# Performance work log

Hardware: AMD Instinct MI355X
Metric: run time of the kernel (lower is better)

The kernel has to match this reference:

```python
import jax, jax.numpy as jnp
import numpy as np

BT, NQ, NC, C, H, HID = 192, 64, 1024, 384, 8, 1536
DH = C // H                       # 48
SCALE = DH ** -0.5
MAX_NEG = -float(np.finfo(np.float32).max)


def _ln(x, eps, g=None, b=None):
    m = x.mean(-1, keepdims=True)
    v = ((x - m) ** 2).mean(-1, keepdims=True)
    y = (x - m) / jnp.sqrt(v + eps)
    if g is not None:
        y = y * g + b
    return y


def _gelu_tanh(x):
    # GELU(approximate='tanh')
    return 0.5 * x * (1.0 + jnp.tanh(jnp.sqrt(2.0 / jnp.pi) * (x + 0.044715 * x ** 3)))


def setup_inputs() -> dict:
    key = jax.random.key(0)
    ks = jax.random.split(key, 10)
    s = lambda fan: 1.0 / np.sqrt(fan)
    return {
        "x": jax.random.normal(ks[0], (BT, NQ, C), jnp.float32),
        "context": jax.random.normal(ks[1], (BT, NC, C), jnp.float32),
        "mask": jax.random.randint(ks[2], (BT, NQ), 0, 2) > 0,
        "Wq": jax.random.normal(ks[3], (C, C), jnp.float32) * s(C),
        "bq": jnp.zeros((C,), jnp.float32),
        "Wkv": jax.random.normal(ks[4], (C, 2 * C), jnp.float32) * s(C),
        "bkv": jnp.zeros((2 * C,), jnp.float32),
        "Wo": jax.random.normal(ks[5], (C, C), jnp.float32) * s(C),
        "bo": jnp.zeros((C,), jnp.float32),
        "g_ctx": jnp.ones((C,), jnp.float32),
        "b_ctx": jnp.zeros((C,), jnp.float32),
        "W1": jax.random.normal(ks[6], (C, HID), jnp.float32) * s(C),
        "b1": jnp.zeros((HID,), jnp.float32),
        "W2": jax.random.normal(ks[7], (HID, C), jnp.float32) * s(HID),
        "b2": jnp.zeros((C,), jnp.float32),
    }


def reference(x, context, mask, Wq, bq, Wkv, bkv, Wo, bo, g_ctx, b_ctx, W1, b1, W2, b2):
    # --- cross-attention branch ---
    xn = _ln(x, 1e-6)                       # norm1 (no affine)
    cn = _ln(context, 1e-5, g_ctx, b_ctx)   # norm_context (affine, default eps)
    q = (xn @ Wq + bq).reshape(BT, NQ, H, DH).transpose(0, 2, 1, 3)    # (B,H,NQ,DH)
    kv = cn @ Wkv + bkv
    k, v = jnp.split(kv, 2, axis=-1)
    k = k.reshape(BT, NC, H, DH).transpose(0, 2, 1, 3)                 # (B,H,NC,DH)
    v = v.reshape(BT, NC, H, DH).transpose(0, 2, 1, 3)
    sim = jnp.einsum('bhqd,bhkd->bhqk', q, k) * SCALE                  # (B,H,NQ,NC)
    # mask shape (BT, NQ): True = keep query row; ~mask * (-max) bias
    bias = jnp.where(mask[:, None, :, None], 0.0, MAX_NEG)
    attn = jax.nn.softmax(sim + bias, axis=-1)
    o = jnp.einsum('bhqk,bhkd->bhqd', attn, v).transpose(0, 2, 1, 3).reshape(BT, NQ, C)
    x = x + o @ Wo + bo
    # --- MLP branch ---
    xn2 = _ln(x, 1e-6)                      # norm2 (no affine)
    x = x + _gelu_tanh(xn2 @ W1 + b1) @ W2 + b2
    return x
```

## Files before the change

kernel.cpp:

```cpp
#include <hip/hip_runtime.h>
#include <hip/hip_bf16.h>
#include <math.h>

typedef unsigned int  u32;
typedef unsigned short u16;
typedef unsigned char u8;

#define BTn   192
#define NQn   64
#define NCn   1024
#define Cd    384
#define Hn    8
#define DHn   48
#define HIDn  1536
#define ROWSX (BTn*NQn)
#define ROWSC (BTn*NCn)
#define ATT_SCALE 0.14433756729740643f
#define CBc   64

typedef __bf16 bf16x8 __attribute__((ext_vector_type(8)));
typedef float  f32x4  __attribute__((ext_vector_type(4)));

#define GLL16(gp, lp) __builtin_amdgcn_global_load_lds( \
    (const __attribute__((address_space(1))) void*)(gp), \
    (__attribute__((address_space(3))) void*)(lp), 16, 0, 0)

__device__ __forceinline__ float bf2f(u32 u) {
  union { u32 i; float f; } v; v.i = u << 16; return v.f;
}
__device__ __forceinline__ u16 f2bf(float f) {
  union { float f; u32 i; } v; v.f = f;
  u32 x = v.i;
  x += 0x7fffu + ((x >> 16) & 1u);
  return (u16)(x >> 16);
}
__device__ __forceinline__ void decode8(uint4 r, float* v) {
  v[0]=bf2f(r.x & 0xffffu); v[1]=bf2f(r.x >> 16);
  v[2]=bf2f(r.y & 0xffffu); v[3]=bf2f(r.y >> 16);
  v[4]=bf2f(r.z & 0xffffu); v[5]=bf2f(r.z >> 16);
  v[6]=bf2f(r.w & 0xffffu); v[7]=bf2f(r.w >> 16);
}
__device__ __forceinline__ float gelu_f(float x) {
  float x3 = x*x*x;
  float z = 0.7978845608028654f*x + 0.035677408136300125f*x3;
  float e = __expf(2.f*z);
  float th = 1.f - 2.f/(e+1.f);
  return 0.5f*x*(1.f+th);
}

__global__ void decode_mask_kernel(const u8* __restrict__ m, u8* __restrict__ keep) {
  __shared__ int flags[3];
  int t = threadIdx.x;
  if (t < 3) flags[t] = 0;
  __syncthreads();
  int nonbin = 0, oddset = 0, low01 = 0;
  for (int i = t; i < ROWSX; i += 256) {
    u32 b = m[i];
    if (b > 1u) nonbin = 1;
    if ((i & 3) && b) oddset = 1;
    if (((i & 3) < 2) && b) low01 = 1;
  }
  if (nonbin) flags[0] = 1;
  if (oddset) flags[1] = 1;
  if (low01)  flags[2] = 1;
  __syncthreads();
  int mode = flags[0] ? (flags[2] ? 2 : 3) : (flags[1] ? 1 : 0);
  for (int i = t; i < ROWSX; i += 256) {
    u8 k;
    if (mode == 2)      k = (m[2*i] | m[2*i+1]) ? 1 : 0;
    else if (mode == 3) k = (((const float*)m)[i] != 0.f) ? 1 : 0;
    else if (mode == 1) k = m[i] ? 1 : 0;
    else                k = (((const int*)m)[i] != 0) ? 1 : 0;
    keep[i] = k;
  }
}

template<int AFF, int SRCF32>
__global__ __launch_bounds__(256) void lnorm_kernel(
    const void* __restrict__ srcv, const float* __restrict__ gw,
    const float* __restrict__ bw, u16* __restrict__ dst, float eps)
{
  const int row  = blockIdx.x * 4 + (threadIdx.x >> 6);
  const int lane = threadIdx.x & 63;
  float v[6];
  if (SRCF32) {
    const float2* p = (const float2*)((const float*)srcv + (size_t)row*Cd);
    #pragma unroll
    for (int i = 0; i < 3; i++) { float2 u = p[lane + 64*i]; v[2*i]=u.x; v[2*i+1]=u.y; }
  } else {
    const u32* p = (const u32*)((const u16*)srcv + (size_t)row*Cd);
    #pragma unroll
    for (int i = 0; i < 3; i++) { u32 u = p[lane + 64*i]; v[2*i]=bf2f(u&0xffffu); v[2*i+1]=bf2f(u>>16); }
  }
  float s  = v[0]+v[1]+v[2]+v[3]+v[4]+v[5];
  float s2 = v[0]*v[0]+v[1]*v[1]+v[2]*v[2]+v[3]*v[3]+v[4]*v[4]+v[5]*v[5];
  #pragma unroll
  for (int o = 32; o >= 1; o >>= 1) { s += __shfl_xor(s, o); s2 += __shfl_xor(s2, o); }
  float mean = s * (1.0f/Cd);
  float var  = s2 * (1.0f/Cd) - mean*mean;
  var = var > 0.f ? var : 0.f;
  float rstd = rsqrtf(var + eps);
  u32* d32 = (u32*)(dst + (size_t)row*Cd);
  #pragma unroll
  for (int i = 0; i < 3; i++) {
    float y0 = (v[2*i]   - mean) * rstd;
    float y1 = (v[2*i+1] - mean) * rstd;
    if (AFF) {
      float2 gg = *(const float2*)(gw + 2*(lane + 64*i));
      float2 bb = *(const float2*)(bw + 2*(lane + 64*i));
      y0 = y0*gg.x + bb.x;
      y1 = y1*gg.y + bb.y;
    }
    d32[lane + 64*i] = (u32)f2bf(y0) | ((u32)f2bf(y1) << 16);
  }
}

__global__ __launch_bounds__(256) void wconvt_kernel(
    const float* __restrict__ W, u16* __restrict__ WT, int K, int N)
{
  __shared__ u16 tile[64][66];
  const int t  = threadIdx.x;
  const int nt = N >> 6;
  const int bk = blockIdx.x / nt, bn = blockIdx.x % nt;
  const int q  = t >> 6;
  const int nl = t & 63;
  #pragma unroll
  for (int r = 0; r < 16; r++) {
    int k = q*16 + r;
    tile[nl][k] = f2bf(W[(size_t)(bk*64 + k)*N + bn*64 + nl]);
  }
  __syncthreads();
  #pragma unroll
  for (int r = 0; r < 16; r++) {
    int n = q*16 + r;
    WT[(size_t)(bn*64 + n)*K + bk*64 + nl] = tile[n][nl];
  }
}

template<int GEL, int RES, int RF32, int OF32>
__global__ __launch_bounds__(256) void mgemm_kernel(
    const u16* __restrict__ A, const u16* __restrict__ WT,
    const float* __restrict__ bias, const void* __restrict__ resv,
    void* __restrict__ Coutv, int M, int N, int K, int nx)
{
  __shared__ u16 As[3][4096];
  __shared__ u16 Bs[3][4096];
  const int t = threadIdx.x;
  const int w = t >> 6, l = t & 63, l15 = l & 15, g = l >> 4;

  const int nwg = gridDim.x;
  const int bid = blockIdx.x;
  const int wg  = (bid & 7) * (nwg >> 3) + (bid >> 3);
  const int n0 = (wg % nx) * 128, m0 = (wg / nx) * 128;
  const int wm = (w & 1) * 64, wn = (w >> 1) * 64;

  const int arow = t >> 2;
  const int swk  = (t >> 3) & 3;
  const int acol = ((t & 3) ^ swk) * 8;
  const u16* Ag = A  + (size_t)(m0 + arow) * K + acol;
  const u16* Wg = WT + (size_t)(n0 + arow) * K + acol;
  const size_t rowskip = (size_t)64 * K;

  const int xk   = (l15 >> 1) & 3;
  const int goff = ((g ^ xk) << 3);

  f32x4 acc[4][4];
  #pragma unroll
  for (int i = 0; i < 4; i++)
    #pragma unroll
    for (int j = 0; j < 4; j++) acc[i][j] = (f32x4){0.f, 0.f, 0.f, 0.f};

  const int nIter = K >> 5;

#define STAGE(nb, kk) do { \
    GLL16(Ag + (kk),           &As[nb][t*8]); \
    GLL16(Ag + (kk) + rowskip, &As[nb][2048 + t*8]); \
    GLL16(Wg + (kk),           &Bs[nb][t*8]); \
    GLL16(Wg + (kk) + rowskip, &Bs[nb][2048 + t*8]); \
  } while (0)

#define BODY(BUF, IT) do { \
    const int it_ = (IT); \
    if (it_ + 2 < nIter) { \
      STAGE((BUF + 2) % 3, (it_ + 2) << 5); \
      asm volatile("s_waitcnt vmcnt(8)" ::: "memory"); \
    } else if (it_ + 1 < nIter) { \
      asm volatile("s_waitcnt vmcnt(4)" ::: "memory"); \
    } else { \
      asm volatile("s_waitcnt vmcnt(0)" ::: "memory"); \
    } \
    __builtin_amdgcn_s_barrier(); \
    __builtin_amdgcn_sched_barrier(0); \
    { \
      bf16x8 af[4], bfv[4]; \
      _Pragma("unroll") \
      for (int i = 0; i < 4; i++) \
        af[i] = *(const bf16x8*)&As[BUF][(wm + i*16 + l15)*32 + goff]; \
      _Pragma("unroll") \
      for (int j = 0; j < 4; j++) \
        bfv[j] = *(const bf16x8*)&Bs[BUF][(wn + j*16 + l15)*32 + goff]; \
      _Pragma("unroll") \
      for (int i = 0; i < 4; i++) \
        _Pragma("unroll") \
        for (int j = 0; j < 4; j++) \
          acc[i][j] = __builtin_amdgcn_mfma_f32_16x16x32_bf16(bfv[j], af[i], acc[i][j], 0, 0, 0); \
    } \
    __builtin_amdgcn_sched_barrier(0); \
    __builtin_amdgcn_s_barrier(); \
  } while (0)

  STAGE(0, 0);
  STAGE(1, 32);
  for (int it0 = 0; it0 < nIter; it0 += 3) {
    BODY(0, it0);
    BODY(1, it0 + 1);
    BODY(2, it0 + 2);
  }
#undef BODY
#undef STAGE

  const float* resf = (const float*)resv;
  const u16*   resb = (const u16*)resv;
  float* Cf = (float*)Coutv;
  u16*   Cb = (u16*)Coutv;
  #pragma unroll
  for (int j = 0; j < 4; j++) {
    const int nb = n0 + wn + j*16 + g*4;
    const float4 bv = *(const float4*)&bias[nb];
    #pragma unroll
    for (int i = 0; i < 4; i++) {
      const int m = m0 + wm + i*16 + l15;
      float c0 = acc[i][j][0] + bv.x;
      float c1 = acc[i][j][1] + bv.y;
      float c2 = acc[i][j][2] + bv.z;
      float c3 = acc[i][j][3] + bv.w;
      if (GEL) { c0 = gelu_f(c0); c1 = gelu_f(c1); c2 = gelu_f(c2); c3 = gelu_f(c3); }
      if (RES) {
        if (RF32) {
          float4 r = *(const float4*)&resf[(size_t)m*N + nb];
          c0 += r.x; c1 += r.y; c2 += r.z; c3 += r.w;
        } else {
          uint2 r = *(const uint2*)&resb[(size_t)m*N + nb];
          c0 += bf2f(r.x & 0xffffu); c1 += bf2f(r.x >> 16);
          c2 += bf2f(r.y & 0xffffu); c3 += bf2f(r.y >> 16);
        }
      }
      if (OF32) {
        *(float4*)&Cf[(size_t)m*N + nb] = make_float4(c0, c1, c2, c3);
      } else {
        uint2 pk = make_uint2((u32)f2bf(c0) | ((u32)f2bf(c1) << 16),
                              (u32)f2bf(c2) | ((u32)f2bf(c3) << 16));
        *(uint2*)&Cb[(size_t)m*N + nb] = pk;
      }
    }
  }
}

__global__ __launch_bounds__(256) void fattn_kernel(
    const u16* __restrict__ qb, const u16* __restrict__ kvb,
    const u8* __restrict__ keep, u16* __restrict__ ob, int b0)
{
  __shared__ u16 Qs[64*72];
  __shared__ u16 Ks[64*72];
  __shared__ u16 Vt[48*72];
  __shared__ u16 Ps[4][16*72];

  const int t = threadIdx.x;
  const int w = t >> 6, l = t & 63, l15 = l & 15, g = l >> 4;
  const int h = blockIdx.x, bz = blockIdx.y;
  const int b = b0 + bz;
  const int wq = w * 16;
  const int krow0 = t / 6, kp0 = t % 6;
  const int krow1 = (256 + t) / 6, kp1 = (256 + t) % 6;
  const int vdq = (t >> 4) * 4, vkq = (t & 15) * 4;

  for (int i = t; i < 2304; i += 256) { ((u32*)Qs)[i] = 0; ((u32*)Ks)[i] = 0; }
  __syncthreads();

  for (int i = t; i < 384; i += 256) {
    int row = i / 6, p = i % 6;
    uint4 v4 = *(const uint4*)(qb + (size_t)(b*NQn + row)*Cd + h*DHn + p*8);
    float f[8]; decode8(v4, f);
    u16 e[8];
    #pragma unroll
    for (int j = 0; j < 8; j++) e[j] = f2bf(f[j] * ATT_SCALE);
    uint4 pk = make_uint4((u32)e[0] | ((u32)e[1] << 16), (u32)e[2] | ((u32)e[3] << 16),
                          (u32)e[4] | ((u32)e[5] << 16), (u32)e[6] | ((u32)e[7] << 16));
    *(uint4*)&Qs[row*72 + p*8] = pk;
  }

  u32 kw = *(const u32*)&keep[b*NQn + wq + g*4];
  float kf[4];
  #pragma unroll
  for (int r = 0; r < 4; r++) kf[r] = ((kw >> (8*r)) & 0xffu) ? 1.f : 0.f;

  float mrow[4], lrow[4];
  f32x4 oacc[3];
  #pragma unroll
  for (int r = 0; r < 4; r++) { mrow[r] = -3.0e38f; lrow[r] = 0.f; }
  #pragma unroll
  for (int d = 0; d < 3; d++) oacc[d] = (f32x4){0.f, 0.f, 0.f, 0.f};

  auto loadKV = [&](int kt, uint4& KR0, uint4& KR1, uint2* V) {
    const u16* base = kvb + ((size_t)bz*NCn + (size_t)kt*64) * (2*(size_t)Cd);
    KR0 = *(const uint4*)(base + (size_t)krow0*(2*Cd) + h*DHn + kp0*8);
    if (t < 128)
      KR1 = *(const uint4*)(base + (size_t)krow1*(2*Cd) + h*DHn + kp1*8);
    if (t < 192) {
      const u16* vs = base + (size_t)vkq*(2*Cd) + Cd + h*DHn + vdq;
      V[0] = *(const uint2*)(vs);
      V[1] = *(const uint2*)(vs + 2*Cd);
      V[2] = *(const uint2*)(vs + 4*Cd);
      V[3] = *(const uint2*)(vs + 6*Cd);
    }
  };
  auto writeKV = [&](const uint4& KR0, const uint4& KR1, const uint2* V) {
    *(uint4*)&Ks[krow0*72 + kp0*8] = KR0;
    if (t < 128) *(uint4*)&Ks[krow1*72 + kp1*8] = KR1;
    if (t < 192) {
      #pragma unroll
      for (int jj = 0; jj < 4; jj++) {
        u16 o4[4] = {((const u16*)&V[0])[jj], ((const u16*)&V[1])[jj],
                     ((const u16*)&V[2])[jj], ((const u16*)&V[3])[jj]};
        *(uint2*)&Vt[(vdq+jj)*72 + vkq] = *(uint2*)o4;
      }
    }
  };

  bf16x8 qf0, qf1;
  auto compute = [&]() {
    f32x4 sf[4];
    #pragma unroll
    for (int f = 0; f < 4; f++) {
      bf16x8 ka = *(const bf16x8*)&Ks[(f*16 + l15)*72 + g*8];
      bf16x8 kb = *(const bf16x8*)&Ks[(f*16 + l15)*72 + 32 + g*8];
      f32x4 z = (f32x4){0.f, 0.f, 0.f, 0.f};
      z = __builtin_amdgcn_mfma_f32_16x16x32_bf16(qf0, ka, z, 0, 0, 0);
      sf[f] = __builtin_amdgcn_mfma_f32_16x16x32_bf16(qf1, kb, z, 0, 0, 0);
    }
    float p[4][4], sc_[4];
    #pragma unroll
    for (int r = 0; r < 4; r++) {
      float pmax = fmaxf(fmaxf(sf[0][r], sf[1][r]), fmaxf(sf[2][r], sf[3][r]));
      #pragma unroll
      for (int s = 1; s < 16; s <<= 1) pmax = fmaxf(pmax, __shfl_xor(pmax, s));
      float mn = kf[r] > 0.f ? fmaxf(mrow[r], pmax) : 0.f;
      sc_[r] = kf[r] > 0.f ? __expf(mrow[r] - mn) : 1.f;
      mrow[r] = mn;
      float p0 = kf[r] > 0.f ? __expf(sf[0][r] - mn) : 1.f;
      float p1 = kf[r] > 0.f ? __expf(sf[1][r] - mn) : 1.f;
      float p2 = kf[r] > 0.f ? __expf(sf[2][r] - mn) : 1.f;
      float p3 = kf[r] > 0.f ? __expf(sf[3][r] - mn) : 1.f;
      p[0][r]=p0; p[1][r]=p1; p[2][r]=p2; p[3][r]=p3;
      float ps = p0+p1+p2+p3;
      #pragma unroll
      for (int s = 1; s < 16; s <<= 1) ps += __shfl_xor(ps, s);
      lrow[r] = lrow[r]*sc_[r] + ps;
      oacc[0][r] *= sc_[r]; oacc[1][r] *= sc_[r]; oacc[2][r] *= sc_[r];
    }
    #pragma unroll
    for (int f = 0; f < 4; f++)
      #pragma unroll
      for (int r = 0; r < 4; r++)
        Ps[w][(g*4 + r)*72 + f*16 + l15] = f2bf(p[f][r]);
    bf16x8 pa0 = *(const bf16x8*)&Ps[w][l15*72 + g*8];
    bf16x8 pa1 = *(const bf16x8*)&Ps[w][l15*72 + 32 + g*8];
    #pragma unroll
    for (int df = 0; df < 3; df++) {
      bf16x8 vb0 = *(const bf16x8*)&Vt[(df*16 + l15)*72 + g*8];
      bf16x8 vb1 = *(const bf16x8*)&Vt[(df*16 + l15)*72 + 32 + g*8];
      oacc[df] = __builtin_amdgcn_mfma_f32_16x16x32_bf16(pa0, vb0, oacc[df], 0, 0, 0);
      oacc[df] = __builtin_amdgcn_mfma_f32_16x16x32_bf16(pa1, vb1, oacc[df], 0, 0, 0);
    }
  };

  uint4 ka0, ka1, kb0_, kb1_;
  uint2 va[4], vb_[4];
  loadKV(0, ka0, ka1, va);
  __syncthreads();

  qf0 = *(const bf16x8*)&Qs[(wq + l15)*72 + g*8];
  qf1 = *(const bf16x8*)&Qs[(wq + l15)*72 + 32 + g*8];

  for (int kt = 0; kt < 16; kt += 2) {
    writeKV(ka0, ka1, va);
    asm volatile("s_waitcnt lgkmcnt(0)" ::: "memory");
    __builtin_amdgcn_sched_barrier(0);
    __builtin_amdgcn_s_barrier();
    __builtin_amdgcn_sched_barrier(0);
    loadKV(kt + 1, kb0_, kb1_, vb_);
    compute();
    __builtin_amdgcn_sched_barrier(0);
    __builtin_amdgcn_s_barrier();
    writeKV(kb0_, kb1_, vb_);
    asm volatile("s_waitcnt lgkmcnt(0)" ::: "memory");
    __builtin_amdgcn_sched_barrier(0);
    __builtin_amdgcn_s_barrier();
    __builtin_amdgcn_sched_barrier(0);
    if (kt + 2 < 16) loadKV(kt + 2, ka0, ka1, va);
    compute();
    if (kt + 2 < 16) {
      __builtin_amdgcn_sched_barrier(0);
      __builtin_amdgcn_s_barrier();
    }
  }

  #pragma unroll
  for (int r = 0; r < 4; r++) {
    float inv = 1.f / lrow[r];
    size_t qrow = (size_t)(b*NQn + wq + g*4 + r);
    #pragma unroll
    for (int df = 0; df < 3; df++)
      ob[qrow*Cd + h*DHn + df*16 + l15] = f2bf(oacc[df][r] * inv);
  }
}

extern "C" void kernel_launch(void* const* d_in, const int* in_sizes, int n_in,
                              void* d_out, int out_size, void* d_ws, size_t ws_size,
                              hipStream_t stream) {
  (void)in_sizes; (void)n_in; (void)out_size; (void)ws_size;
  const float* x   = (const float*)d_in[0];
  const float* ctx = (const float*)d_in[1];
  const u8*    msk = (const u8*)   d_in[2];
  const float* Wq  = (const float*)d_in[3];
  const float* bq  = (const float*)d_in[4];
  const float* Wkv = (const float*)d_in[5];
  const float* bkv = (const float*)d_in[6];
  const float* Wo  = (const float*)d_in[7];
  const float* bo  = (const float*)d_in[8];
  const float* gc  = (const float*)d_in[9];
  const float* bc  = (const float*)d_in[10];
  const float* W1  = (const float*)d_in[11];
  const float* b1  = (const float*)d_in[12];
  const float* W2  = (const float*)d_in[13];
  const float* b2  = (const float*)d_in[14];
  float* out = (float*)d_out;

  char* ws = (char*)d_ws;
  size_t off = 0;
  auto bump = [&](size_t bytes) -> size_t {
    size_t o = off; off += (bytes + 255) & ~(size_t)255; return o;
  };
  const size_t act = (size_t)ROWSX * Cd * 2;
  size_t o_keep = bump(ROWSX);
  size_t o_xn   = bump(act);
  size_t o_x1n  = bump(act);
  size_t o_q    = bump(act);
  size_t o_ob   = bump(act);
  size_t o_x1   = bump(act);
  size_t o_hid  = bump((size_t)4096 * HIDn * 2);
  size_t o_wtq  = bump((size_t)Cd*Cd*2);
  size_t o_wtkv = bump((size_t)Cd*2*Cd*2);
  size_t o_wto  = bump((size_t)Cd*Cd*2);
  size_t o_wt1  = bump((size_t)Cd*HIDn*2);
  size_t o_wt2  = bump((size_t)HIDn*Cd*2);
  size_t o_cn   = bump((size_t)CBc * NCn * Cd * 2);
  size_t o_kv   = bump((size_t)CBc * NCn * 2 * Cd * 2);

  u8*  keep = (u8*)(ws + o_keep);
  u16* xn   = (u16*)(ws + o_xn);
  u16* x1n  = (u16*)(ws + o_x1n);
  u16* qb   = (u16*)(ws + o_q);
  u16* obuf = (u16*)(ws + o_ob);
  u16* x1b  = (u16*)(ws + o_x1);
  u16* hidb = (u16*)(ws + o_hid);
  u16* wtq  = (u16*)(ws + o_wtq);
  u16* wtkv = (u16*)(ws + o_wtkv);
  u16* wto  = (u16*)(ws + o_wto);
  u16* wt1  = (u16*)(ws + o_wt1);
  u16* wt2  = (u16*)(ws + o_wt2);
  u16* cnb  = (u16*)(ws + o_cn);
  u16* kvb  = (u16*)(ws + o_kv);

  decode_mask_kernel<<<1, 256, 0, stream>>>(msk, keep);

  wconvt_kernel<<<(Cd/64)*(Cd/64),     256, 0, stream>>>(Wq,  wtq,  Cd,   Cd);
  wconvt_kernel<<<(Cd/64)*(2*Cd/64),   256, 0, stream>>>(Wkv, wtkv, Cd,   2*Cd);
  wconvt_kernel<<<(Cd/64)*(Cd/64),     256, 0, stream>>>(Wo,  wto,  Cd,   Cd);
  wconvt_kernel<<<(Cd/64)*(HIDn/64),   256, 0, stream>>>(W1,  wt1,  Cd,   HIDn);
  wconvt_kernel<<<(HIDn/64)*(Cd/64),   256, 0, stream>>>(W2,  wt2,  HIDn, Cd);

  lnorm_kernel<0,1><<<ROWSX/4, 256, 0, stream>>>(x, nullptr, nullptr, xn, 1e-6f);

  mgemm_kernel<0,0,0,0><<<3*(ROWSX/128), 256, 0, stream>>>(
      xn, wtq, bq, nullptr, qb, ROWSX, Cd, Cd, 3);

  for (int b0 = 0; b0 < BTn; b0 += CBc) {
    lnorm_kernel<1,1><<<CBc*NCn/4, 256, 0, stream>>>(
        ctx + (size_t)b0*NCn*Cd, gc, bc, cnb, 1e-5f);
    mgemm_kernel<0,0,0,0><<<6*(CBc*NCn/128), 256, 0, stream>>>(
        cnb, wtkv, bkv, nullptr, kvb, CBc*NCn, 2*Cd, Cd, 6);
    fattn_kernel<<<dim3(Hn, CBc), 256, 0, stream>>>(qb, kvb, keep, obuf, b0);
  }

  mgemm_kernel<0,1,1,0><<<3*(ROWSX/128), 256, 0, stream>>>(
      obuf, wto, bo, x, x1b, ROWSX, Cd, Cd, 3);

  lnorm_kernel<0,0><<<ROWSX/4, 256, 0, stream>>>(x1b, nullptr, nullptr, x1n, 1e-6f);

  for (int rc = 0; rc < 3; rc++) {
    const size_t r0 = (size_t)rc * 4096;
    mgemm_kernel<1,0,0,0><<<12*(4096/128), 256, 0, stream>>>(
        x1n + r0*Cd, wt1, b1, nullptr, hidb, 4096, HIDn, Cd, 12);
    mgemm_kernel<0,1,0,1><<<3*(4096/128), 256, 0, stream>>>(
        hidb, wt2, b2, x1b + r0*Cd, out + r0*Cd, 4096, Cd, HIDn, 3);
  }
}
```

Baseline: 667.5 us.

## Add 128x256 triple-buffered GEMM for KV and MLP1, merge weight conversions, unchunk MLP

Adds a 512-thread GEMM kernel with 128x256 tiles, three-stage LDS buffering and an XCD-aware block swizzle. It is used for the context KV projection and the first MLP layer, aiming for more operand reuse per tile and better overlap of loads with MFMA. The five weight-transpose launches become one packed launch, and the MLP now runs over all rows at once instead of in three chunks, which needs a larger hidden buffer. The bigger tiles give fewer workgroups and more LDS and register pressure per block.

```diff
diff --git a/kernel.cpp b/kernel.cpp
--- a/kernel.cpp
+++ b/kernel.cpp
@@ -115,13 +115,26 @@
   }
 }
 
-__global__ __launch_bounds__(256) void wconvt_kernel(
-    const float* __restrict__ W, u16* __restrict__ WT, int K, int N)
-{
+struct WPack {
+  const float* W[5];
+  u16* WT[5];
+  int K[5];
+  int N[5];
+  int off[6];
+};
+__global__ __launch_bounds__(256) void wconvt_all_kernel(WPack p) {
   __shared__ u16 tile[64][66];
+  const int bid = blockIdx.x;
+  int s = 0;
+  #pragma unroll
+  for (int i = 1; i < 5; i++) if (bid >= p.off[i]) s = i;
+  const float* W = p.W[s];
+  u16* WT = p.WT[s];
+  const int K = p.K[s], N = p.N[s];
+  const int lb = bid - p.off[s];
   const int t  = threadIdx.x;
   const int nt = N >> 6;
-  const int bk = blockIdx.x / nt, bn = blockIdx.x % nt;
+  const int bk = lb / nt, bn = lb % nt;
   const int q  = t >> 6;
   const int nl = t & 63;
   #pragma unroll
@@ -256,6 +269,124 @@
   }
 }
 
+template<int GEL, int RES, int RF32, int OF32>
+__global__ __launch_bounds__(512, 4) void mgemm256_kernel(
+    const u16* __restrict__ A, const u16* __restrict__ WT,
+    const float* __restrict__ bias, const void* __restrict__ resv,
+    void* __restrict__ Coutv, int M, int N, int K, int nx)
+{
+  __shared__ u16 As[3][4096];
+  __shared__ u16 Bs[3][8192];
+  const int t = threadIdx.x;
+  const int w = t >> 6, l = t & 63, l15 = l & 15, g = l >> 4;
+
+  const int nwg = gridDim.x;
+  const int bid = blockIdx.x;
+  const int wg  = (bid & 7) * (nwg >> 3) + (bid >> 3);
+  const int n0 = (wg % nx) * 256, m0 = (wg / nx) * 128;
+  const int wm = (w & 1) * 64, wn = (w >> 1) * 64;
+
+  const int arow = t >> 2;
+  const int swk  = (t >> 3) & 3;
+  const int acol = ((t & 3) ^ swk) * 8;
+  const u16* Ag = A  + (size_t)(m0 + arow) * K + acol;
+  const u16* Wg = WT + (size_t)(n0 + arow) * K + acol;
+  const size_t rowskipB = (size_t)128 * K;
+
+  const int xk   = (l15 >> 1) & 3;
+  const int goff = ((g ^ xk) << 3);
+
+  f32x4 acc[4][4];
+  #pragma unroll
+  for (int i = 0; i < 4; i++)
+    #pragma unroll
+    for (int j = 0; j < 4; j++) acc[i][j] = (f32x4){0.f, 0.f, 0.f, 0.f};
+
+  const int nIter = K >> 5;
+
+#define STAGE(nb, kk) do { \
+    GLL16(Ag + (kk),            &As[nb][t*8]); \
+    GLL16(Wg + (kk),            &Bs[nb][t*8]); \
+    GLL16(Wg + (kk) + rowskipB, &Bs[nb][4096 + t*8]); \
+  } while (0)
+
+#define BODY(BUF, IT) do { \
+    const int it_ = (IT); \
+    if (it_ + 2 < nIter) { \
+      STAGE((BUF + 2) % 3, (it_ + 2) << 5); \
+      asm volatile("s_waitcnt vmcnt(6)" ::: "memory"); \
+    } else if (it_ + 1 < nIter) { \
+      asm volatile("s_waitcnt vmcnt(3)" ::: "memory"); \
+    } else { \
+      asm volatile("s_waitcnt vmcnt(0)" ::: "memory"); \
+    } \
+    __builtin_amdgcn_s_barrier(); \
+    __builtin_amdgcn_sched_barrier(0); \
+    { \
+      bf16x8 af[4], bfv[4]; \
+      _Pragma("unroll") \
+      for (int i = 0; i < 4; i++) \
+        af[i] = *(const bf16x8*)&As[BUF][(wm + i*16 + l15)*32 + goff]; \
+      _Pragma("unroll") \
+      for (int j = 0; j < 4; j++) \
+        bfv[j] = *(const bf16x8*)&Bs[BUF][(wn + j*16 + l15)*32 + goff]; \
+      _Pragma("unroll") \
+      for (int i = 0; i < 4; i++) \
+        _Pragma("unroll") \
+        for (int j = 0; j < 4; j++) \
+          acc[i][j] = __builtin_amdgcn_mfma_f32_16x16x32_bf16(bfv[j], af[i], acc[i][j], 0, 0, 0); \
+    } \
+    __builtin_amdgcn_sched_barrier(0); \
+    __builtin_amdgcn_s_barrier(); \
+  } while (0)
+
+  STAGE(0, 0);
+  STAGE(1, 32);
+  for (int it0 = 0; it0 < nIter; it0 += 3) {
+    BODY(0, it0);
+    BODY(1, it0 + 1);
+    BODY(2, it0 + 2);
+  }
+#undef BODY
+#undef STAGE
+
+  const float* resf = (const float*)resv;
+  const u16*   resb = (const u16*)resv;
+  float* Cf = (float*)Coutv;
+  u16*   Cb = (u16*)Coutv;
+  #pragma unroll
+  for (int j = 0; j < 4; j++) {
+    const int nb = n0 + wn + j*16 + g*4;
+    const float4 bv = *(const float4*)&bias[nb];
+    #pragma unroll
+    for (int i = 0; i < 4; i++) {
+      const int m = m0 + wm + i*16 + l15;
+      float c0 = acc[i][j][0] + bv.x;
+      float c1 = acc[i][j][1] + bv.y;
+      float c2 = acc[i][j][2] + bv.z;
+      float c3 = acc[i][j][3] + bv.w;
+      if (GEL) { c0 = gelu_f(c0); c1 = gelu_f(c1); c2 = gelu_f(c2); c3 = gelu_f(c3); }
+      if (RES) {
+        if (RF32) {
+          float4 r = *(const float4*)&resf[(size_t)m*N + nb];
+          c0 += r.x; c1 += r.y; c2 += r.z; c3 += r.w;
+        } else {
+          uint2 r = *(const uint2*)&resb[(size_t)m*N + nb];
+          c0 += bf2f(r.x & 0xffffu); c1 += bf2f(r.x >> 16);
+          c2 += bf2f(r.y & 0xffffu); c3 += bf2f(r.y >> 16);
+        }
+      }
+      if (OF32) {
+        *(float4*)&Cf[(size_t)m*N + nb] = make_float4(c0, c1, c2, c3);
+      } else {
+        uint2 pk = make_uint2((u32)f2bf(c0) | ((u32)f2bf(c1) << 16),
+                              (u32)f2bf(c2) | ((u32)f2bf(c3) << 16));
+        *(uint2*)&Cb[(size_t)m*N + nb] = pk;
+      }
+    }
+  }
+}
+
 __global__ __launch_bounds__(256) void fattn_kernel(
     const u16* __restrict__ qb, const u16* __restrict__ kvb,
     const u8* __restrict__ keep, u16* __restrict__ ob, int b0)
@@ -448,7 +579,7 @@
   size_t o_q    = bump(act);
   size_t o_ob   = bump(act);
   size_t o_x1   = bump(act);
-  size_t o_hid  = bump((size_t)4096 * HIDn * 2);
+  size_t o_hid  = bump((size_t)ROWSX * HIDn * 2);
   size_t o_wtq  = bump((size_t)Cd*Cd*2);
   size_t o_wtkv = bump((size_t)Cd*2*Cd*2);
   size_t o_wto  = bump((size_t)Cd*Cd*2);
@@ -474,11 +605,14 @@
 
   decode_mask_kernel<<<1, 256, 0, stream>>>(msk, keep);
 
-  wconvt_kernel<<<(Cd/64)*(Cd/64),     256, 0, stream>>>(Wq,  wtq,  Cd,   Cd);
-  wconvt_kernel<<<(Cd/64)*(2*Cd/64),   256, 0, stream>>>(Wkv, wtkv, Cd,   2*Cd);
-  wconvt_kernel<<<(Cd/64)*(Cd/64),     256, 0, stream>>>(Wo,  wto,  Cd,   Cd);
-  wconvt_kernel<<<(Cd/64)*(HIDn/64),   256, 0, stream>>>(W1,  wt1,  Cd,   HIDn);
-  wconvt_kernel<<<(HIDn/64)*(Cd/64),   256, 0, stream>>>(W2,  wt2,  HIDn, Cd);
+  WPack wp;
+  wp.W[0]=Wq;  wp.WT[0]=wtq;  wp.K[0]=Cd;   wp.N[0]=Cd;
+  wp.W[1]=Wkv; wp.WT[1]=wtkv; wp.K[1]=Cd;   wp.N[1]=2*Cd;
+  wp.W[2]=Wo;  wp.WT[2]=wto;  wp.K[2]=Cd;   wp.N[2]=Cd;
+  wp.W[3]=W1;  wp.WT[3]=wt1;  wp.K[3]=Cd;   wp.N[3]=HIDn;
+  wp.W[4]=W2;  wp.WT[4]=wt2;  wp.K[4]=HIDn; wp.N[4]=Cd;
+  wp.off[0]=0; wp.off[1]=36; wp.off[2]=108; wp.off[3]=144; wp.off[4]=288; wp.off[5]=432;
+  wconvt_all_kernel<<<432, 256, 0, stream>>>(wp);
 
   lnorm_kernel<0,1><<<ROWSX/4, 256, 0, stream>>>(x, nullptr, nullptr, xn, 1e-6f);
 
@@ -488,8 +622,8 @@
   for (int b0 = 0; b0 < BTn; b0 += CBc) {
     lnorm_kernel<1,1><<<CBc*NCn/4, 256, 0, stream>>>(
         ctx + (size_t)b0*NCn*Cd, gc, bc, cnb, 1e-5f);
-    mgemm_kernel<0,0,0,0><<<6*(CBc*NCn/128), 256, 0, stream>>>(
-        cnb, wtkv, bkv, nullptr, kvb, CBc*NCn, 2*Cd, Cd, 6);
+    mgemm256_kernel<0,0,0,0><<<3*(CBc*NCn/128), 512, 0, stream>>>(
+        cnb, wtkv, bkv, nullptr, kvb, CBc*NCn, 2*Cd, Cd, 3);
     fattn_kernel<<<dim3(Hn, CBc), 256, 0, stream>>>(qb, kvb, keep, obuf, b0);
   }
 
@@ -498,11 +632,9 @@
 
   lnorm_kernel<0,0><<<ROWSX/4, 256, 0, stream>>>(x1b, nullptr, nullptr, x1n, 1e-6f);
 
-  for (int rc = 0; rc < 3; rc++) {
-    const size_t r0 = (size_t)rc * 4096;
-    mgemm_kernel<1,0,0,0><<<12*(4096/128), 256, 0, stream>>>(
-        x1n + r0*Cd, wt1, b1, nullptr, hidb, 4096, HIDn, Cd, 12);
-    mgemm_kernel<0,1,0,1><<<3*(4096/128), 256, 0, stream>>>(
-        hidb, wt2, b2, x1b + r0*Cd, out + r0*Cd, 4096, Cd, HIDn, 3);
-  }
-}
+  mgemm256_kernel<1,0,0,0><<<6*(ROWSX/128), 512, 0, stream>>>(
+      x1n, wt1, b1, nullptr, hidb, ROWSX, HIDn, Cd, 6);
+
+  mgemm_kernel<0,1,0,1><<<3*(ROWSX/128), 256, 0, stream>>>(
+      hidb, wt2, b2, x1b, out, ROWSX, Cd, HIDn, 3);
+}
```

New measurement: 574.2 us. -14.0%, faster.
